# Performance work log

Measured on AMD Instinct MI355X. Metric: run time of the kernel, lower is better.

Reference implementation:

```python
import jax, jax.numpy as jnp
import numpy as np

EPS = 1e-5

def _bn(x, g, b):
    m = x.mean(axis=0)
    v = x.var(axis=0)  # biased, matches torch BN training normalization
    return g * (x - m) * jax.lax.rsqrt(v + EPS) + b

def _mlp(x, W1, b1, g1, be1, W2, b2, g2, be2):
    h = jax.nn.relu(_bn(x @ W1 + b1, g1, be1))
    return jax.nn.relu(_bn(h @ W2 + b2, g2, be2))

def setup_inputs() -> dict:
    key = jax.random.key(0)
    ks = jax.random.split(key, 12)
    n, e, d, de = 100000, 1600000, 128, 16
    def lin(k, fan_in, fan_out):
        bound = 1.0 / np.sqrt(fan_in)
        k1, k2 = jax.random.split(k)
        W = jax.random.uniform(k1, (fan_in, fan_out), jnp.float32, -bound, bound)
        b = jax.random.uniform(k2, (fan_out,), jnp.float32, -bound, bound)
        return W, b
    msg_W1, msg_b1 = lin(ks[0], 2 * d + de, d)
    msg_W2, msg_b2 = lin(ks[1], d, d)
    upd_W1, upd_b1 = lin(ks[2], 3 * d, d)
    upd_W2, upd_b2 = lin(ks[3], d, d)
    return {
        "h": jax.random.normal(ks[4], (n, d), jnp.float32),
        "edge_index": jax.random.randint(ks[5], (2, e), 0, n, jnp.int64),
        "edge_attr": jax.random.normal(ks[6], (e, de), jnp.float32),
        "msg_W1": msg_W1, "msg_b1": msg_b1,
        "msg_g1": jnp.ones((d,)), "msg_be1": jnp.zeros((d,)),
        "msg_W2": msg_W2, "msg_b2": msg_b2,
        "msg_g2": jnp.ones((d,)), "msg_be2": jnp.zeros((d,)),
        "upd_W1": upd_W1, "upd_b1": upd_b1,
        "upd_g1": jnp.ones((d,)), "upd_be1": jnp.zeros((d,)),
        "upd_W2": upd_W2, "upd_b2": upd_b2,
        "upd_g2": jnp.ones((d,)), "upd_be2": jnp.zeros((d,)),
    }

def reference(h, edge_index, edge_attr,
              msg_W1, msg_b1, msg_g1, msg_be1, msg_W2, msg_b2, msg_g2, msg_be2,
              upd_W1, upd_b1, upd_g1, upd_be1, upd_W2, upd_b2, upd_g2, upd_be2):
    alpha = 0.5
    n = h.shape[0]
    src = edge_index[0]
    dst = edge_index[1]
    h_i = h[src]  # (e, d)
    h_j = h[dst]  # (e, d)
    msg_args = (msg_W1, msg_b1, msg_g1, msg_be1, msg_W2, msg_b2, msg_g2, msg_be2)
    m_st = _mlp(jnp.concatenate([h_i, h_j, edge_attr], axis=-1), *msg_args)
    m_ts = _mlp(jnp.concatenate([h_j, h_i, edge_attr], axis=-1), *msg_args)
    # NOTE: original code scatters both directions by source nodes (faithful)
    a_st = jax.ops.segment_sum(m_st, src, num_segments=n)
    a_ts = jax.ops.segment_sum(m_ts, src, num_segments=n)
    upd_in = jnp.concatenate([h, alpha * a_st, (1.0 - alpha) * a_ts], axis=-1)
    return _mlp(upd_in, upd_W1, upd_b1, upd_g1, upd_be1, upd_W2, upd_b2, upd_g2, upd_be2)
```

## Files before the change

kernel.cpp:

```cpp
#include <hip/hip_runtime.h>

#define EPS_BN 1e-5f

typedef __bf16 bf16x8 __attribute__((ext_vector_type(8)));
typedef float f32x4 __attribute__((ext_vector_type(4)));
typedef unsigned short us8 __attribute__((ext_vector_type(8)));
typedef unsigned short us4 __attribute__((ext_vector_type(4)));
typedef unsigned int u32x4 __attribute__((ext_vector_type(4)));

__device__ __forceinline__ unsigned short f2bf(float x) {
  unsigned u = __builtin_bit_cast(unsigned, x);
  unsigned r = (u + 0x7fffu + ((u >> 16) & 1u)) >> 16;
  return (unsigned short)r;
}
__device__ __forceinline__ unsigned pack2bf(float a, float b) {
  return (unsigned)f2bf(a) | ((unsigned)f2bf(b) << 16);
}
__device__ __forceinline__ unsigned long long pack4bf(float a, float b, float c, float d) {
  return (unsigned long long)pack2bf(a, b) | ((unsigned long long)pack2bf(c, d) << 32);
}
__device__ __forceinline__ float ubf(unsigned short u) {
  return __builtin_bit_cast(float, (unsigned)u << 16);
}

__device__ __forceinline__ int fragidx(int k, int c) {
  int nf = c >> 4, lr = c & 15, ks = k >> 5, lq = (k >> 3) & 3, j = k & 7;
  return ((((nf << 2) + ks) << 6) | (lq << 4) | lr) * 8 + j;
}

__global__ __launch_bounds__(256) void prep_all(
    const float* __restrict__ mW1, const float* __restrict__ mW2,
    const float* __restrict__ uW1, const float* __restrict__ uW2,
    unsigned short* __restrict__ wfrag) {
  int b = blockIdx.x;
  const float* src;
  float sc = 1.f;
  switch (b) {
    case 0: src = mW1; break;
    case 1: src = mW1 + 16384; break;
    case 2: src = mW2; break;
    case 3: src = uW1; break;
    case 4: src = uW1 + 16384; sc = 0.5f; break;
    case 5: src = uW1 + 32768; sc = 0.5f; break;
    default: src = uW2; break;
  }
  unsigned short* oc = wfrag + (long)b * 16384;
  for (int i = threadIdx.x; i < 16384; i += 256) {
    oc[fragidx(i >> 7, i & 127)] = f2bf(src[i] * sc);
  }
}

__global__ __launch_bounds__(256) void node_mfma_pq(
    const float* __restrict__ h, const unsigned short* __restrict__ WfA,
    unsigned short* __restrict__ pqb, int n) {
  __shared__ unsigned short WT[16384];
  int tid = threadIdx.x;
  int lid = tid & 63, w = tid >> 6, lr = lid & 15, lq = lid >> 4;
  long rbase = (long)blockIdx.x * 64 + 16 * w;
  long r = rbase + lr;
  bool rv = (r < n);
  long rl = rv ? r : 0;
  const us8* WF8 = (const us8*)WT;

  bf16x8 af[4];
  const float* Ar = h + rl * 128;
  #pragma unroll
  for (int ks = 0; ks < 4; ++ks) {
    int e0 = 32 * ks + 8 * lq;
    float4 x = *(const float4*)(Ar + e0);
    float4 y = *(const float4*)(Ar + e0 + 4);
    u32x4 t;
    t[0] = pack2bf(x.x, x.y); t[1] = pack2bf(x.z, x.w);
    t[2] = pack2bf(y.x, y.y); t[3] = pack2bf(y.z, y.w);
    if (!rv) { t[0] = 0; t[1] = 0; t[2] = 0; t[3] = 0; }
    af[ks] = __builtin_bit_cast(bf16x8, t);
  }

  f32x4 accP[8], accQ[8];
  #pragma unroll
  for (int nf = 0; nf < 8; ++nf) {
    accP[nf] = f32x4{0.f, 0.f, 0.f, 0.f};
    accQ[nf] = f32x4{0.f, 0.f, 0.f, 0.f};
  }

  for (int i = tid; i < 2048; i += 256) ((us8*)WT)[i] = ((const us8*)WfA)[i];
  __syncthreads();
  #pragma unroll
  for (int nf = 0; nf < 8; ++nf) {
    #pragma unroll
    for (int ks = 0; ks < 4; ++ks) {
      bf16x8 bf = __builtin_bit_cast(bf16x8, WF8[(nf * 4 + ks) * 64 + lid]);
      accP[nf] = __builtin_amdgcn_mfma_f32_16x16x32_bf16(af[ks], bf, accP[nf], 0, 0, 0);
    }
  }
  __syncthreads();
  for (int i = tid; i < 2048; i += 256) ((us8*)WT)[i] = ((const us8*)(WfA + 16384))[i];
  __syncthreads();
  #pragma unroll
  for (int nf = 0; nf < 8; ++nf) {
    #pragma unroll
    for (int ks = 0; ks < 4; ++ks) {
      bf16x8 bf = __builtin_bit_cast(bf16x8, WF8[(nf * 4 + ks) * 64 + lid]);
      accQ[nf] = __builtin_amdgcn_mfma_f32_16x16x32_bf16(af[ks], bf, accQ[nf], 0, 0, 0);
    }
  }

  #pragma unroll
  for (int nf = 0; nf < 8; ++nf) {
    #pragma unroll
    for (int i = 0; i < 4; ++i) {
      long nd = rbase + 4 * lq + i;
      if (nd < n) {
        int ch = 16 * nf + lr;
        pqb[nd * 256 + ch] = f2bf(accP[nf][i]);
        pqb[nd * 256 + 128 + ch] = f2bf(accQ[nf][i]);
      }
    }
  }
}

template <bool ABF16>
__global__ __launch_bounds__(256) void node_mfma(
    const void* A0, const void* A1, const void* A2,
    const unsigned short* __restrict__ Wf,
    float* __restrict__ C, int n, int dostats,
    float* __restrict__ sum_out, float* __restrict__ ssq_out, int nk) {
  __shared__ unsigned short WT[16384];
  int tid = threadIdx.x;
  int lid = tid & 63, w = tid >> 6, lr = lid & 15, lq = lid >> 4;
  long rbase = (long)blockIdx.x * 64 + 16 * w;

  const void* As[3] = {A0, A1, A2};
  f32x4 acc[8];
  #pragma unroll
  for (int nf = 0; nf < 8; ++nf) acc[nf] = f32x4{0.f, 0.f, 0.f, 0.f};

  long r = rbase + lr;
  bool rv = (r < n);
  long rl = rv ? r : 0;
  const us8* WF8 = (const us8*)WT;

  for (int c = 0; c < nk; ++c) {
    if (c) __syncthreads();
    const us8* src = (const us8*)(Wf + (long)c * 16384);
    for (int i = tid; i < 2048; i += 256) ((us8*)WT)[i] = src[i];
    __syncthreads();

    bf16x8 af[4];
    if (ABF16) {
      const us8* Ar = (const us8*)((const unsigned short*)As[c] + rl * 128);
      #pragma unroll
      for (int ks = 0; ks < 4; ++ks) {
        us8 v = Ar[ks * 4 + lq];
        if (!rv) v = us8{0, 0, 0, 0, 0, 0, 0, 0};
        af[ks] = __builtin_bit_cast(bf16x8, v);
      }
    } else {
      const float* Ar = (const float*)As[c] + rl * 128;
      #pragma unroll
      for (int ks = 0; ks < 4; ++ks) {
        int e0 = 32 * ks + 8 * lq;
        float4 x = *(const float4*)(Ar + e0);
        float4 y = *(const float4*)(Ar + e0 + 4);
        u32x4 t;
        t[0] = pack2bf(x.x, x.y); t[1] = pack2bf(x.z, x.w);
        t[2] = pack2bf(y.x, y.y); t[3] = pack2bf(y.z, y.w);
        if (!rv) { t[0] = 0; t[1] = 0; t[2] = 0; t[3] = 0; }
        af[ks] = __builtin_bit_cast(bf16x8, t);
      }
    }
    #pragma unroll
    for (int nf = 0; nf < 8; ++nf) {
      #pragma unroll
      for (int ks = 0; ks < 4; ++ks) {
        bf16x8 bf = __builtin_bit_cast(bf16x8, WF8[(nf * 4 + ks) * 64 + lid]);
        acc[nf] = __builtin_amdgcn_mfma_f32_16x16x32_bf16(af[ks], bf, acc[nf], 0, 0, 0);
      }
    }
  }

  float lsum[8], lssq[8];
  #pragma unroll
  for (int nf = 0; nf < 8; ++nf) { lsum[nf] = 0.f; lssq[nf] = 0.f; }
  #pragma unroll
  for (int nf = 0; nf < 8; ++nf) {
    #pragma unroll
    for (int i = 0; i < 4; ++i) {
      long nd = rbase + 4 * lq + i;
      if (nd < n) {
        float v = acc[nf][i];
        C[nd * 128 + 16 * nf + lr] = v;
        lsum[nf] += v; lssq[nf] += v * v;
      }
    }
  }
  if (dostats) {
    #pragma unroll
    for (int nf = 0; nf < 8; ++nf) {
      float v0 = lsum[nf]; v0 += __shfl_xor(v0, 16); v0 += __shfl_xor(v0, 32);
      float v1 = lssq[nf]; v1 += __shfl_xor(v1, 16); v1 += __shfl_xor(v1, 32);
      if (lq == 0) {
        atomicAdd(&sum_out[16 * nf + lr], v0);
        atomicAdd(&ssq_out[16 * nf + lr], v1);
      }
    }
  }
}

__global__ __launch_bounds__(256) void msg_stats1b(
    const unsigned short* __restrict__ PQ,
    const float* __restrict__ EA, const float* __restrict__ W1e,
    const int* __restrict__ SRC, const int* __restrict__ DST, long E,
    float* __restrict__ stats) {
  __shared__ float Wel[16][128];
  __shared__ float red[32][16];
  int tid = threadIdx.x;
  for (int i = tid; i < 16 * 128; i += 256) ((float*)Wel)[i] = W1e[i];
  for (int i = tid; i < 512; i += 256) ((float*)red)[i] = 0.f;
  __syncthreads();
  int c4 = tid & 31, grp = tid >> 5;
  float4 s_st = {0,0,0,0}, q_st = {0,0,0,0}, s_ts = {0,0,0,0}, q_ts = {0,0,0,0};
  long stride = (long)gridDim.x * 8;
  for (long e = (long)blockIdx.x * 8 + grp; e < E; e += stride) {
    int s = SRC[e], t = DST[e];
    const unsigned short* Rs = PQ + (long)s * 256;
    const unsigned short* Rt = PQ + (long)t * 256;
    us4 Ps = *(const us4*)(Rs + 4 * c4);
    us4 Qs = *(const us4*)(Rs + 128 + 4 * c4);
    us4 Pt = *(const us4*)(Rt + 4 * c4);
    us4 Qt = *(const us4*)(Rt + 128 + 4 * c4);
    float rx = 0.f, ry = 0.f, rz = 0.f, rw = 0.f;
    const float* eap = EA + e * 16;
    #pragma unroll
    for (int k = 0; k < 16; ++k) {
      float f = eap[k];
      const float4 w4 = *(const float4*)&Wel[k][c4 * 4];
      rx = fmaf(f, w4.x, rx); ry = fmaf(f, w4.y, ry);
      rz = fmaf(f, w4.z, rz); rw = fmaf(f, w4.w, rw);
    }
    float zx = ubf(Ps[0]) + ubf(Qt[0]) + rx, zy = ubf(Ps[1]) + ubf(Qt[1]) + ry;
    float zz = ubf(Ps[2]) + ubf(Qt[2]) + rz, zw = ubf(Ps[3]) + ubf(Qt[3]) + rw;
    s_st.x += zx; s_st.y += zy; s_st.z += zz; s_st.w += zw;
    q_st.x += zx * zx; q_st.y += zy * zy; q_st.z += zz * zz; q_st.w += zw * zw;
    float ux = ubf(Pt[0]) + ubf(Qs[0]) + rx, uy = ubf(Pt[1]) + ubf(Qs[1]) + ry;
    float uz = ubf(Pt[2]) + ubf(Qs[2]) + rz, uw = ubf(Pt[3]) + ubf(Qs[3]) + rw;
    s_ts.x += ux; s_ts.y += uy; s_ts.z += uz; s_ts.w += uw;
    q_ts.x += ux * ux; q_ts.y += uy * uy; q_ts.z += uz * uz; q_ts.w += uw * uw;
  }
  atomicAdd(&red[c4][0], s_st.x);  atomicAdd(&red[c4][1], s_st.y);
  atomicAdd(&red[c4][2], s_st.z);  atomicAdd(&red[c4][3], s_st.w);
  atomicAdd(&red[c4][4], q_st.x);  atomicAdd(&red[c4][5], q_st.y);
  atomicAdd(&red[c4][6], q_st.z);  atomicAdd(&red[c4][7], q_st.w);
  atomicAdd(&red[c4][8], s_ts.x);  atomicAdd(&red[c4][9], s_ts.y);
  atomicAdd(&red[c4][10], s_ts.z); atomicAdd(&red[c4][11], s_ts.w);
  atomicAdd(&red[c4][12], q_ts.x); atomicAdd(&red[c4][13], q_ts.y);
  atomicAdd(&red[c4][14], q_ts.z); atomicAdd(&red[c4][15], q_ts.w);
  __syncthreads();
  #pragma unroll
  for (int rep = 0; rep < 2; ++rep) {
    int j = rep * 256 + tid;
    int cc = j >> 4, k = j & 15, group = k >> 2, comp = k & 3;
    atomicAdd(&stats[group * 128 + cc * 4 + comp], red[cc][k]);
  }
}

template <bool SCATTER>
__global__ __launch_bounds__(256) void msg_mfma3(
    const unsigned short* __restrict__ PQ,
    const float* __restrict__ EA, const float* __restrict__ W1e,
    const unsigned short* __restrict__ W2f,
    const int* __restrict__ SRC, const int* __restrict__ DST, long E,
    const float* __restrict__ sc1, const float* __restrict__ sc2,
    float* __restrict__ stats2,
    float* __restrict__ a_st, float* __restrict__ a_ts) {
  __shared__ float Wel[16][128];
  __shared__ unsigned short W2F[16384];
  __shared__ unsigned short Ast[64][136];
  __shared__ unsigned short Ats[64][136];
  __shared__ int sArr[64];

  int tid = threadIdx.x;
  int c4 = tid & 31;
  int slot = tid >> 5;
  int lid = tid & 63;
  int w = tid >> 6;
  int lr = lid & 15;
  int lq = lid >> 4;

  for (int i = tid; i < 16 * 128; i += 256) ((float*)Wel)[i] = W1e[i];
  for (int i = tid; i < 2048; i += 256) ((us8*)W2F)[i] = ((const us8*)W2f)[i];
  const us8* W2F8 = (const us8*)W2F;

  const float4* sc1v = (const float4*)sc1;
  float4 scst = sc1v[c4], shst = sc1v[32 + c4];
  float4 scts = sc1v[64 + c4], shts = sc1v[96 + c4];

  float s2st[8], h2st[8], s2ts[8], h2ts[8];
  if constexpr (SCATTER) {
    #pragma unroll
    for (int nf = 0; nf < 8; ++nf) {
      int ch = 16 * nf + lr;
      s2st[nf] = sc2[ch];       h2st[nf] = sc2[128 + ch];
      s2ts[nf] = sc2[256 + ch]; h2ts[nf] = sc2[384 + ch];
    }
  }
  float ssum_st[8], sssq_st[8], ssum_ts[8], sssq_ts[8];
  if constexpr (!SCATTER) {
    #pragma unroll
    for (int nf = 0; nf < 8; ++nf) {
      ssum_st[nf] = 0.f; sssq_st[nf] = 0.f; ssum_ts[nf] = 0.f; sssq_ts[nf] = 0.f;
    }
  }
  __syncthreads();

  for (long tb = (long)blockIdx.x * 64; tb < E; tb += (long)gridDim.x * 64) {
    int nE = (int)(E - tb < 64 ? E - tb : 64);

    #pragma unroll 2
    for (int rep = 0; rep < 8; ++rep) {
      int er = rep * 8 + slot;
      if (er < nE) {
        long e = tb + er;
        int s = SRC[e], t = DST[e];
        if (SCATTER && c4 == 0) sArr[er] = s;
        const us4* Rs = (const us4*)(PQ + (long)s * 256);
        const us4* Rt = (const us4*)(PQ + (long)t * 256);
        us4 Ps = Rs[c4];
        us4 Qs = Rs[32 + c4];
        us4 Pt = Rt[c4];
        us4 Qt = Rt[32 + c4];
        float rx = 0.f, ry = 0.f, rz = 0.f, rw = 0.f;
        const float* eap = EA + e * 16;
        #pragma unroll
        for (int k = 0; k < 16; ++k) {
          float f = eap[k];
          const float4 w4 = *(const float4*)&Wel[k][c4 * 4];
          rx = fmaf(f, w4.x, rx); ry = fmaf(f, w4.y, ry);
          rz = fmaf(f, w4.z, rz); rw = fmaf(f, w4.w, rw);
        }
        float ax = fmaxf(fmaf(ubf(Ps[0]) + ubf(Qt[0]) + rx, scst.x, shst.x), 0.f);
        float ay = fmaxf(fmaf(ubf(Ps[1]) + ubf(Qt[1]) + ry, scst.y, shst.y), 0.f);
        float az = fmaxf(fmaf(ubf(Ps[2]) + ubf(Qt[2]) + rz, scst.z, shst.z), 0.f);
        float aw = fmaxf(fmaf(ubf(Ps[3]) + ubf(Qt[3]) + rw, scst.w, shst.w), 0.f);
        *(unsigned long long*)&Ast[er][c4 * 4] = pack4bf(ax, ay, az, aw);
        float bx = fmaxf(fmaf(ubf(Pt[0]) + ubf(Qs[0]) + rx, scts.x, shts.x), 0.f);
        float by = fmaxf(fmaf(ubf(Pt[1]) + ubf(Qs[1]) + ry, scts.y, shts.y), 0.f);
        float bz = fmaxf(fmaf(ubf(Pt[2]) + ubf(Qs[2]) + rz, scts.z, shts.z), 0.f);
        float bw = fmaxf(fmaf(ubf(Pt[3]) + ubf(Qs[3]) + rw, scts.w, shts.w), 0.f);
        *(unsigned long long*)&Ats[er][c4 * 4] = pack4bf(bx, by, bz, bw);
      } else {
        *(unsigned long long*)&Ast[er][c4 * 4] = 0ull;
        *(unsigned long long*)&Ats[er][c4 * 4] = 0ull;
      }
    }
    __syncthreads();

    int arow = 16 * w + lr;
    const char* astp = (const char*)&Ast[arow][0];
    const char* atsp = (const char*)&Ats[arow][0];
    int acolb = lq * 16;
    bf16x8 afst[4], afts[4];
    #pragma unroll
    for (int ks = 0; ks < 4; ++ks) {
      afst[ks] = *(const bf16x8*)(astp + ks * 64 + acolb);
      afts[ks] = *(const bf16x8*)(atsp + ks * 64 + acolb);
    }
    int srow[4];
    if constexpr (SCATTER) {
      #pragma unroll
      for (int i = 0; i < 4; ++i) {
        int row = 16 * w + 4 * lq + i;
        srow[i] = (row < nE) ? sArr[row] : -1;
      }
    }
    #pragma unroll
    for (int nf = 0; nf < 8; ++nf) {
      f32x4 acc_st = {0.f, 0.f, 0.f, 0.f};
      f32x4 acc_ts = {0.f, 0.f, 0.f, 0.f};
      #pragma unroll
      for (int ks = 0; ks < 4; ++ks) {
        bf16x8 bf = __builtin_bit_cast(bf16x8, W2F8[(nf * 4 + ks) * 64 + lid]);
        acc_st = __builtin_amdgcn_mfma_f32_16x16x32_bf16(afst[ks], bf, acc_st, 0, 0, 0);
        acc_ts = __builtin_amdgcn_mfma_f32_16x16x32_bf16(afts[ks], bf, acc_ts, 0, 0, 0);
      }
      if constexpr (SCATTER) {
        int ch = 16 * nf + lr;
        #pragma unroll
        for (int i = 0; i < 4; ++i) {
          if (srow[i] >= 0) {
            float m1 = fmaxf(fmaf(acc_st[i], s2st[nf], h2st[nf]), 0.f);
            float m2 = fmaxf(fmaf(acc_ts[i], s2ts[nf], h2ts[nf]), 0.f);
            if (m1 > 0.f) atomicAdd(&a_st[(long)srow[i] * 128 + ch], m1);
            if (m2 > 0.f) atomicAdd(&a_ts[(long)srow[i] * 128 + ch], m2);
          }
        }
      } else {
        #pragma unroll
        for (int i = 0; i < 4; ++i) {
          ssum_st[nf] += acc_st[i]; sssq_st[nf] += acc_st[i] * acc_st[i];
          ssum_ts[nf] += acc_ts[i]; sssq_ts[nf] += acc_ts[i] * acc_ts[i];
        }
      }
    }
    __syncthreads();
  }

  if constexpr (!SCATTER) {
    #pragma unroll
    for (int nf = 0; nf < 8; ++nf) {
      float v0 = ssum_st[nf]; v0 += __shfl_xor(v0, 16); v0 += __shfl_xor(v0, 32);
      float v1 = sssq_st[nf]; v1 += __shfl_xor(v1, 16); v1 += __shfl_xor(v1, 32);
      float v2 = ssum_ts[nf]; v2 += __shfl_xor(v2, 16); v2 += __shfl_xor(v2, 32);
      float v3 = sssq_ts[nf]; v3 += __shfl_xor(v3, 16); v3 += __shfl_xor(v3, 32);
      if (lq == 0) {
        int ch = 16 * nf + lr;
        atomicAdd(&stats2[ch], v0);
        atomicAdd(&stats2[128 + ch], v1);
        atomicAdd(&stats2[256 + ch], v2);
        atomicAdd(&stats2[384 + ch], v3);
      }
    }
  }
}

__global__ void bn_finalize(const float* __restrict__ sum, const float* __restrict__ ssq,
                            float invN, const float* __restrict__ g,
                            const float* __restrict__ be,
                            float* __restrict__ sc, float* __restrict__ sh) {
  int j = threadIdx.x;
  float m = sum[j] * invN;
  float v = ssq[j] * invN - m * m;
  float s = g[j] * rsqrtf(v + EPS_BN);
  sc[j] = s;
  sh[j] = be[j] - m * s;
}

__global__ __launch_bounds__(256) void prescale_relu(
    const float* __restrict__ X, const float* __restrict__ scsh,
    unsigned* __restrict__ out, long nrows) {
  long gid = (long)blockIdx.x * 256 + threadIdx.x;
  int c2 = (int)(gid & 63);
  float s0 = scsh[2 * c2], s1 = scsh[2 * c2 + 1];
  float h0 = scsh[128 + 2 * c2], h1 = scsh[128 + 2 * c2 + 1];
  const float2* X2 = (const float2*)X;
  long rstride = ((long)gridDim.x * 256) >> 6;
  for (long row = gid >> 6; row < nrows; row += rstride) {
    float2 x = X2[row * 64 + c2];
    out[row * 64 + c2] = pack2bf(fmaxf(fmaf(x.x, s0, h0), 0.f),
                                 fmaxf(fmaf(x.y, s1, h1), 0.f));
  }
}

__global__ __launch_bounds__(256) void bn_relu_out(
    const float* __restrict__ U2, const float* __restrict__ scsh,
    float* __restrict__ out, long total) {
  long i = (long)blockIdx.x * blockDim.x + threadIdx.x;
  long stride = (long)gridDim.x * blockDim.x;
  for (; i < total; i += stride) {
    int j = (int)(i & 127);
    out[i] = fmaxf(fmaf(U2[i], scsh[j], scsh[128 + j]), 0.f);
  }
}

extern "C" void kernel_launch(void* const* d_in, const int* in_sizes, int n_in,
                              void* d_out, int out_size, void* d_ws, size_t ws_size,
                              hipStream_t stream) {
  const float* h    = (const float*)d_in[0];
  const int*   ei   = (const int*)d_in[1];
  const float* ea   = (const float*)d_in[2];
  const float* mW1  = (const float*)d_in[3];
  const float* mg1  = (const float*)d_in[5];
  const float* mbe1 = (const float*)d_in[6];
  const float* mW2  = (const float*)d_in[7];
  const float* mg2  = (const float*)d_in[9];
  const float* mbe2 = (const float*)d_in[10];
  const float* uW1  = (const float*)d_in[11];
  const float* ug1  = (const float*)d_in[13];
  const float* ube1 = (const float*)d_in[14];
  const float* uW2  = (const float*)d_in[15];
  const float* ug2  = (const float*)d_in[17];
  const float* ube2 = (const float*)d_in[18];

  int n = in_sizes[0] / 128;
  long E = (long)(in_sizes[1] / 2);
  const int* SRC = ei;
  const int* DST = ei + E;
  const float* W1e = mW1 + 256 * 128;

  size_t nf = (size_t)n * 128;
  unsigned short* pqb = (unsigned short*)d_ws;
  float* a_st = (float*)(pqb + (size_t)n * 256);
  float* a_ts = a_st + nf;
  float* st   = a_ts + nf;
  unsigned short* wfrag = (unsigned short*)(st + 3072);
  unsigned short* wfA  = wfrag;
  unsigned short* wfW2 = wfrag + 2 * 16384;
  unsigned short* wfU1 = wfrag + 3 * 16384;
  unsigned short* wfU2 = wfrag + 6 * 16384;

  float invE = 1.0f / (float)E;
  float invN = 1.0f / (float)n;
  int nblk = (n + 63) / 64;

  prep_all<<<7, 256, 0, stream>>>(mW1, mW2, uW1, uW2, wfrag);
  hipMemsetAsync(st, 0, 3072 * sizeof(float), stream);
  hipMemsetAsync(a_st, 0, 2 * nf * sizeof(float), stream);

  node_mfma_pq<<<nblk, 256, 0, stream>>>(h, wfA, pqb, n);

  msg_stats1b<<<2048, 256, 0, stream>>>(pqb, ea, W1e, SRC, DST, E, st);
  bn_finalize<<<1, 128, 0, stream>>>(st + 0,   st + 128, invE, mg1, mbe1, st + 1536, st + 1664);
  bn_finalize<<<1, 128, 0, stream>>>(st + 256, st + 384, invE, mg1, mbe1, st + 1792, st + 1920);

  msg_mfma3<false><<<1024, 256, 0, stream>>>(
      pqb, ea, W1e, wfW2, SRC, DST, E, st + 1536, nullptr, st + 512, nullptr, nullptr);
  bn_finalize<<<1, 128, 0, stream>>>(st + 512, st + 640, invE, mg2, mbe2, st + 2048, st + 2176);
  bn_finalize<<<1, 128, 0, stream>>>(st + 768, st + 896, invE, mg2, mbe2, st + 2304, st + 2432);

  msg_mfma3<true><<<1024, 256, 0, stream>>>(
      pqb, ea, W1e, wfW2, SRC, DST, E, st + 1536, st + 2048, nullptr, a_st, a_ts);

  float* u1 = (float*)pqb;
  node_mfma<false><<<nblk, 256, 0, stream>>>(h, a_st, a_ts, wfU1,
                                             u1, n, 1, st + 1024, st + 1152, 3);
  bn_finalize<<<1, 128, 0, stream>>>(st + 1024, st + 1152, invN, ug1, ube1, st + 2560, st + 2688);

  unsigned short* u1p = (unsigned short*)a_st;
  float* u2 = a_ts;
  prescale_relu<<<2048, 256, 0, stream>>>(u1, st + 2560, (unsigned*)u1p, n);
  node_mfma<true><<<nblk, 256, 0, stream>>>(u1p, nullptr, nullptr, wfU2,
                                            u2, n, 1, st + 1280, st + 1408, 1);
  bn_finalize<<<1, 128, 0, stream>>>(st + 1280, st + 1408, invN, ug2, ube2, st + 2816, st + 2944);

  bn_relu_out<<<2048, 256, 0, stream>>>(u2, st + 2816, (float*)d_out, (long)n * 128);
}
```

Before: 2.675 ms.

## Sort edges by source via counting sort and merge scatter atomics per row

Adds a histogram, prefix scan and permute pass that reorders edges by source node and stores edge attributes as bf16. The three edge passes then read the sorted indices and the half-size attributes, and the scatter merges consecutive same-source rows within each MFMA fragment before issuing atomics. This is meant to cut atomic traffic and improve locality of the source gathers and a_st/a_ts writes. The cost is five extra kernels with one pass of atomics, more workspace, and a bf16 rounding of edge attributes before the first linear layer.

```diff
diff --git a/kernel.cpp b/kernel.cpp
--- a/kernel.cpp
+++ b/kernel.cpp
@@ -50,6 +50,90 @@
   }
 }
 
+__global__ __launch_bounds__(256) void hist_kernel(
+    const int* __restrict__ SRC, long E, int* __restrict__ counts) {
+  long i = (long)blockIdx.x * 256 + threadIdx.x;
+  long str = (long)gridDim.x * 256;
+  for (; i < E; i += str) atomicAdd(&counts[SRC[i]], 1);
+}
+
+__global__ __launch_bounds__(256) void scan1(
+    const int* __restrict__ counts, int n, int* __restrict__ tmp,
+    int* __restrict__ bsum) {
+  __shared__ int sd[256];
+  int b = blockIdx.x, tid = threadIdx.x;
+  int base = b * 1024 + tid * 4;
+  int c[4], t = 0;
+  #pragma unroll
+  for (int j = 0; j < 4; ++j) {
+    int idx = base + j;
+    c[j] = (idx < n) ? counts[idx] : 0;
+    t += c[j];
+  }
+  sd[tid] = t;
+  __syncthreads();
+  for (int off = 1; off < 256; off <<= 1) {
+    int v = (tid >= off) ? sd[tid - off] : 0;
+    __syncthreads();
+    sd[tid] += v;
+    __syncthreads();
+  }
+  int run = sd[tid] - t;
+  #pragma unroll
+  for (int j = 0; j < 4; ++j) {
+    int idx = base + j;
+    if (idx < n) tmp[idx] = run;
+    run += c[j];
+  }
+  if (tid == 255) bsum[b] = sd[255];
+}
+
+__global__ __launch_bounds__(256) void scan2(int* __restrict__ bsum, int nb) {
+  __shared__ int sd[256];
+  int tid = threadIdx.x;
+  int v = (tid < nb) ? bsum[tid] : 0;
+  sd[tid] = v;
+  __syncthreads();
+  for (int off = 1; off < 256; off <<= 1) {
+    int x = (tid >= off) ? sd[tid - off] : 0;
+    __syncthreads();
+    sd[tid] += x;
+    __syncthreads();
+  }
+  if (tid < nb) bsum[tid] = sd[tid] - v;
+}
+
+__global__ __launch_bounds__(256) void scan3(
+    const int* __restrict__ tmp, const int* __restrict__ bsum, int n,
+    int* __restrict__ cursor) {
+  int i = blockIdx.x * 256 + threadIdx.x;
+  if (i < n) cursor[i] = tmp[i] + bsum[i >> 10];
+}
+
+__global__ __launch_bounds__(256) void permute_edges(
+    const int* __restrict__ SRC, const int* __restrict__ DST,
+    const float* __restrict__ EA, long E, int* __restrict__ cursor,
+    int* __restrict__ sS, int* __restrict__ sD,
+    unsigned short* __restrict__ EAb) {
+  long i = (long)blockIdx.x * 256 + threadIdx.x;
+  long str = (long)gridDim.x * 256;
+  for (; i < E; i += str) {
+    int s = SRC[i];
+    int pos = atomicAdd(&cursor[s], 1);
+    sS[pos] = s;
+    sD[pos] = DST[i];
+    const float4* ep = (const float4*)(EA + i * 16);
+    float4 a = ep[0], b = ep[1], c = ep[2], d = ep[3];
+    u32x4 lo, hi;
+    lo[0] = pack2bf(a.x, a.y); lo[1] = pack2bf(a.z, a.w);
+    lo[2] = pack2bf(b.x, b.y); lo[3] = pack2bf(b.z, b.w);
+    hi[0] = pack2bf(c.x, c.y); hi[1] = pack2bf(c.z, c.w);
+    hi[2] = pack2bf(d.x, d.y); hi[3] = pack2bf(d.z, d.w);
+    *(u32x4*)(EAb + (long)pos * 16) = lo;
+    *(u32x4*)(EAb + (long)pos * 16 + 8) = hi;
+  }
+}
+
 __global__ __launch_bounds__(256) void node_mfma_pq(
     const float* __restrict__ h, const unsigned short* __restrict__ WfA,
     unsigned short* __restrict__ pqb, int n) {
@@ -209,7 +293,7 @@
 
 __global__ __launch_bounds__(256) void msg_stats1b(
     const unsigned short* __restrict__ PQ,
-    const float* __restrict__ EA, const float* __restrict__ W1e,
+    const unsigned short* __restrict__ EAb, const float* __restrict__ W1e,
     const int* __restrict__ SRC, const int* __restrict__ DST, long E,
     float* __restrict__ stats) {
   __shared__ float Wel[16][128];
@@ -229,11 +313,12 @@
     us4 Qs = *(const us4*)(Rs + 128 + 4 * c4);
     us4 Pt = *(const us4*)(Rt + 4 * c4);
     us4 Qt = *(const us4*)(Rt + 128 + 4 * c4);
+    us8 evlo = *(const us8*)(EAb + e * 16);
+    us8 evhi = *(const us8*)(EAb + e * 16 + 8);
     float rx = 0.f, ry = 0.f, rz = 0.f, rw = 0.f;
-    const float* eap = EA + e * 16;
     #pragma unroll
     for (int k = 0; k < 16; ++k) {
-      float f = eap[k];
+      float f = (k < 8) ? ubf(evlo[k & 7]) : ubf(evhi[k & 7]);
       const float4 w4 = *(const float4*)&Wel[k][c4 * 4];
       rx = fmaf(f, w4.x, rx); ry = fmaf(f, w4.y, ry);
       rz = fmaf(f, w4.z, rz); rw = fmaf(f, w4.w, rw);
@@ -265,9 +350,9 @@
 }
 
 template <bool SCATTER>
-__global__ __launch_bounds__(256) void msg_mfma3(
+__global__ __launch_bounds__(256) void msg_mfma5(
     const unsigned short* __restrict__ PQ,
-    const float* __restrict__ EA, const float* __restrict__ W1e,
+    const unsigned short* __restrict__ EAb, const float* __restrict__ W1e,
     const unsigned short* __restrict__ W2f,
     const int* __restrict__ SRC, const int* __restrict__ DST, long E,
     const float* __restrict__ sc1, const float* __restrict__ sc2,
@@ -329,11 +414,12 @@
         us4 Qs = Rs[32 + c4];
         us4 Pt = Rt[c4];
         us4 Qt = Rt[32 + c4];
+        us8 evlo = *(const us8*)(EAb + e * 16);
+        us8 evhi = *(const us8*)(EAb + e * 16 + 8);
         float rx = 0.f, ry = 0.f, rz = 0.f, rw = 0.f;
-        const float* eap = EA + e * 16;
         #pragma unroll
         for (int k = 0; k < 16; ++k) {
-          float f = eap[k];
+          float f = (k < 8) ? ubf(evlo[k & 7]) : ubf(evhi[k & 7]);
           const float4 w4 = *(const float4*)&Wel[k][c4 * 4];
           rx = fmaf(f, w4.x, rx); ry = fmaf(f, w4.y, ry);
           rz = fmaf(f, w4.z, rz); rw = fmaf(f, w4.w, rw);
@@ -385,14 +471,26 @@
       }
       if constexpr (SCATTER) {
         int ch = 16 * nf + lr;
+        int cur = srow[0];
+        float m1 = fmaxf(fmaf(acc_st[0], s2st[nf], h2st[nf]), 0.f);
+        float m2 = fmaxf(fmaf(acc_ts[0], s2ts[nf], h2ts[nf]), 0.f);
         #pragma unroll
-        for (int i = 0; i < 4; ++i) {
-          if (srow[i] >= 0) {
-            float m1 = fmaxf(fmaf(acc_st[i], s2st[nf], h2st[nf]), 0.f);
-            float m2 = fmaxf(fmaf(acc_ts[i], s2ts[nf], h2ts[nf]), 0.f);
-            if (m1 > 0.f) atomicAdd(&a_st[(long)srow[i] * 128 + ch], m1);
-            if (m2 > 0.f) atomicAdd(&a_ts[(long)srow[i] * 128 + ch], m2);
+        for (int i = 1; i < 4; ++i) {
+          float v1 = fmaxf(fmaf(acc_st[i], s2st[nf], h2st[nf]), 0.f);
+          float v2 = fmaxf(fmaf(acc_ts[i], s2ts[nf], h2ts[nf]), 0.f);
+          if (srow[i] == cur) {
+            m1 += v1; m2 += v2;
+          } else {
+            if (cur >= 0) {
+              if (m1 != 0.f) atomicAdd(&a_st[(long)cur * 128 + ch], m1);
+              if (m2 != 0.f) atomicAdd(&a_ts[(long)cur * 128 + ch], m2);
+            }
+            cur = srow[i]; m1 = v1; m2 = v2;
           }
+        }
+        if (cur >= 0) {
+          if (m1 != 0.f) atomicAdd(&a_st[(long)cur * 128 + ch], m1);
+          if (m2 != 0.f) atomicAdd(&a_ts[(long)cur * 128 + ch], m2);
         }
       } else {
         #pragma unroll
@@ -497,28 +595,42 @@
   unsigned short* wfW2 = wfrag + 2 * 16384;
   unsigned short* wfU1 = wfrag + 3 * 16384;
   unsigned short* wfU2 = wfrag + 6 * 16384;
+  int* sS = (int*)(wfrag + 7 * 16384);
+  int* sD = sS + E;
+  unsigned short* EAb = (unsigned short*)(sD + E);
+  int* counts = (int*)(EAb + (size_t)E * 16);
+  int* tmp = counts + n;
+  int* bsum = tmp + n;
 
   float invE = 1.0f / (float)E;
   float invN = 1.0f / (float)n;
   int nblk = (n + 63) / 64;
+  int nb1 = (n + 1023) / 1024;
 
   prep_all<<<7, 256, 0, stream>>>(mW1, mW2, uW1, uW2, wfrag);
   hipMemsetAsync(st, 0, 3072 * sizeof(float), stream);
   hipMemsetAsync(a_st, 0, 2 * nf * sizeof(float), stream);
+  hipMemsetAsync(counts, 0, (size_t)n * sizeof(int), stream);
+
+  hist_kernel<<<1024, 256, 0, stream>>>(SRC, E, counts);
+  scan1<<<nb1, 256, 0, stream>>>(counts, n, tmp, bsum);
+  scan2<<<1, 256, 0, stream>>>(bsum, nb1);
+  scan3<<<(n + 255) / 256, 256, 0, stream>>>(tmp, bsum, n, counts);
+  permute_edges<<<1024, 256, 0, stream>>>(SRC, DST, ea, E, counts, sS, sD, EAb);
 
   node_mfma_pq<<<nblk, 256, 0, stream>>>(h, wfA, pqb, n);
 
-  msg_stats1b<<<2048, 256, 0, stream>>>(pqb, ea, W1e, SRC, DST, E, st);
+  msg_stats1b<<<2048, 256, 0, stream>>>(pqb, EAb, W1e, sS, sD, E, st);
   bn_finalize<<<1, 128, 0, stream>>>(st + 0,   st + 128, invE, mg1, mbe1, st + 1536, st + 1664);
   bn_finalize<<<1, 128, 0, stream>>>(st + 256, st + 384, invE, mg1, mbe1, st + 1792, st + 1920);
 
-  msg_mfma3<false><<<1024, 256, 0, stream>>>(
-      pqb, ea, W1e, wfW2, SRC, DST, E, st + 1536, nullptr, st + 512, nullptr, nullptr);
+  msg_mfma5<false><<<1024, 256, 0, stream>>>(
+      pqb, EAb, W1e, wfW2, sS, sD, E, st + 1536, nullptr, st + 512, nullptr, nullptr);
   bn_finalize<<<1, 128, 0, stream>>>(st + 512, st + 640, invE, mg2, mbe2, st + 2048, st + 2176);
   bn_finalize<<<1, 128, 0, stream>>>(st + 768, st + 896, invE, mg2, mbe2, st + 2304, st + 2432);
 
-  msg_mfma3<true><<<1024, 256, 0, stream>>>(
-      pqb, ea, W1e, wfW2, SRC, DST, E, st + 1536, st + 2048, nullptr, a_st, a_ts);
+  msg_mfma5<true><<<1024, 256, 0, stream>>>(
+      pqb, EAb, W1e, wfW2, sS, sD, E, st + 1536, st + 2048, nullptr, a_st, a_ts);
 
   float* u1 = (float*)pqb;
   node_mfma<false><<<nblk, 256, 0, stream>>>(h, a_st, a_ts, wfU1,
```

After: 2.600 ms. 1.03x faster.
